# Kernel tuning notes

Measured on AMD Instinct MI355X. Metric: run time of the kernel, lower is better.

Reference implementation:

```python
import math
import jax, jax.numpy as jnp
from jax import lax
import numpy as np

BSZ, NQ, L, DM, DI, H, HD, DDIST, DCONV, DHID = 2, 128, 2048, 256, 512, 8, 64, 16, 4, 64
DKEY = DI * 2 + 2 + H  # key_proj output: z + xbc + per-head dt bias
DCV = DI + 2           # depthwise conv channels


def setup_inputs() -> dict:
    key = jax.random.key(0)
    ks = jax.random.split(key, 40)
    it = iter(range(40))
    def n(shape, s=1.0):
        return jax.random.normal(ks[next(it)], shape, jnp.float32) * s
    # dt_bias init exactly as in torch module
    dt = jnp.exp(jax.random.uniform(ks[next(it)], (H,)) * (math.log(0.1) - math.log(0.001)) + math.log(0.001))
    dt = jnp.maximum(dt, 1e-4)
    dt_bias = dt + jnp.log(-jnp.expm1(-dt))
    A_log = jnp.log(jax.random.uniform(ks[next(it)], (H,), minval=1.0, maxval=16.0))
    return {
        'queries': n((BSZ, NQ, DM)), 'anchors': n((BSZ, NQ, 3), 10.0),
        'features_perm': n((BSZ, L, DM)), 'pos_embed_perm': n((BSZ, L, DM)),
        'key_pos_3d': n((BSZ, L, 3), 10.0), 'query_pos': n((BSZ, NQ, DM)),
        'key_proj_w': n((DM, DKEY), 0.02),
        'key_conv_w': n((DCV, DCONV), 0.1), 'key_conv_b': jnp.zeros((DCV,)),
        'query_proj_w': n((DM, DI), 0.02),
        'dist_w1': n((3, DHID), 0.3), 'dist_b1': jnp.zeros((DHID,)), 'dist_w2': n((DHID, DDIST), 0.1),
        'bc_proj_w': n((DDIST, 2), 0.2), 'dt_proj_w': n((DDIST, H), 0.2),
        'dt_bias': dt_bias, 'A_log': A_log, 'D': jnp.ones((H,)),
        'key_norm_w': jnp.ones((DI,)), 'out_key_proj_w': n((DI, DM), 0.02),
        'query_norm_w': jnp.ones((DI,)), 'query_norm_b': jnp.zeros((DI,)),
        'out_query_proj_w': n((DI, DM), 0.02),
        'ffn_norm_w': jnp.ones((DM,)), 'ffn_norm_b': jnp.zeros((DM,)),
        'ffn_fc1_w': n((DM, 8 * DM), 0.02), 'ffn_fc1_b': jnp.zeros((8 * DM,)),
        'ffn_fc2_w': n((4 * DM, DM), 0.02), 'ffn_fc2_b': jnp.zeros((DM,)),
    }


def _ln(x, w, b, eps=1e-5):
    m = jnp.mean(x, -1, keepdims=True)
    v = jnp.mean((x - m) ** 2, -1, keepdims=True)
    return (x - m) * lax.rsqrt(v + eps) * w + b


def _dwconv_causal(x, w, b):
    # x [B,L,C], w [C,K]; torch pads K-1 both sides then slices [:L] == causal left pad
    lhs = jnp.swapaxes(x, 1, 2)  # [B,C,L]
    out = lax.conv_general_dilated(lhs, w[:, None, :], (1,), [(DCONV - 1, 0)],
                                   feature_group_count=w.shape[0],
                                   dimension_numbers=('NCH', 'OIH', 'NCH'))
    return jnp.swapaxes(out + b[None, :, None], 1, 2)


def _issm(x, dt, A, Bs, Cs, Dp, init):
    # x [B,L,H,P]; dt [B,L,H,N]; A [H,N]; Bs/Cs [B,L,N]; init [B,H,P,N]
    def step(h, inp):
        xt, dtt, bt, ct = inp  # [B,H,P], [B,H,N], [B,N], [B,N]
        h = h * jnp.exp(dtt * A)[:, :, None, :] + (dtt * bt[:, None, :])[:, :, None, :] * xt[..., None]
        return h, jnp.einsum('bhpn,bn->bhp', h, ct)
    xs = (jnp.swapaxes(x, 0, 1), jnp.swapaxes(dt, 0, 1), jnp.swapaxes(Bs, 0, 1), jnp.swapaxes(Cs, 0, 1))
    h_last, ys = lax.scan(step, init, xs)
    y = jnp.swapaxes(ys, 0, 1) + x * Dp[None, None, :, None]  # D skip inside scan, as in ISSM_chunk_scan_combined
    return y, h_last


def _forward(queries, anchors, features_perm, pos_embed_perm, key_pos_3d, query_pos,
             key_proj_w, key_conv_w, key_conv_b, query_proj_w, dist_w1, dist_b1, dist_w2,
             bc_proj_w, dt_proj_w, dt_bias, A_log, D, key_norm_w, out_key_proj_w,
             query_norm_w, query_norm_b, out_query_proj_w, ffn_norm_w, ffn_norm_b,
             ffn_fc1_w, ffn_fc1_b, ffn_fc2_w, ffn_fc2_b):
    qp = queries + query_pos
    kp = (features_perm + pos_embed_perm) @ key_proj_w            # [B,L,DKEY]
    z, xbc, dtb_seq = kp[..., :DI], kp[..., DI:DI + DCV], kp[..., DI + DCV:]
    xbc = jax.nn.silu(_dwconv_causal(xbc, key_conv_w, key_conv_b))
    x = xbc[..., :DI]
    b_bias, c_bias = xbc[..., DI], xbc[..., DI + 1]               # [B,L]
    init = (qp @ query_proj_w).reshape(BSZ, NQ, H, HD).transpose(0, 2, 3, 1)  # [B,H,HD,NQ]
    # distance features: delta [B,L,NQ,3]
    delta = anchors[:, None, :, :] - key_pos_3d[:, :, None, :]
    enc = jnp.sign(delta) * jnp.log2(jnp.abs(delta) * 20.0 + 1.0) / math.log2(8.0) / 4.0
    feat = jax.nn.relu(enc @ dist_w1 + dist_b1) @ dist_w2         # [B,L,NQ,DDIST]
    bc = feat @ bc_proj_w                                         # [B,L,NQ,2]
    Bssm = bc[..., 0] + b_bias[..., None]                         # [B,L,NQ]
    Cssm = bc[..., 1] + c_bias[..., None]
    dtb = jnp.swapaxes(feat @ dt_proj_w, 2, 3)                    # [B,L,H,NQ]
    dt = jax.nn.softplus(dtb + dtb_seq[..., None] + dt_bias[None, None, :, None])
    A = jnp.broadcast_to(-jnp.exp(A_log)[:, None], (H, NQ))
    xs = x.reshape(BSZ, L, H, HD)
    y_f, h_f = _issm(xs, dt, A, Bssm, Cssm, D, init)
    fl = lambda a: jnp.flip(a, axis=1)
    y_b, h_b = _issm(fl(xs), fl(dt), A, fl(Bssm), fl(Cssm), D, init)
    y = (y_f + fl(y_b)) * 0.5
    h = (h_f + h_b) * 0.5                                         # [B,H,HD,NQ]
    y = y.reshape(BSZ, L, DI) + x * jnp.repeat(D, HD)[None, None, :]
    # gated RMSNorm (norm_before_gate=False): gate first, then normalize
    g = y * jax.nn.silu(z)
    g = g * lax.rsqrt(jnp.mean(g * g, -1, keepdims=True) + 1e-5) * key_norm_w
    out_feat = features_perm + g @ out_key_proj_w
    hs = h.transpose(0, 3, 1, 2).reshape(BSZ, NQ, DI)             # b h hd n -> b n (h hd)
    out_q = queries + _ln(hs, query_norm_w, query_norm_b) @ out_query_proj_w
    fn = _ln(out_q, ffn_norm_w, ffn_norm_b)
    a, v = jnp.split(fn @ ffn_fc1_w + ffn_fc1_b, 2, axis=-1)
    out_q = out_q + (jax.nn.gelu(a, approximate=False) * v) @ ffn_fc2_w + ffn_fc2_b
    return out_q, out_feat


def reference(queries, anchors, features_perm, pos_embed_perm, key_pos_3d, query_pos,
              key_proj_w, key_conv_w, key_conv_b, query_proj_w, dist_w1, dist_b1, dist_w2,
              bc_proj_w, dt_proj_w, dt_bias, A_log, D, key_norm_w, out_key_proj_w,
              query_norm_w, query_norm_b, out_query_proj_w, ffn_norm_w, ffn_norm_b,
              ffn_fc1_w, ffn_fc1_b, ffn_fc2_w, ffn_fc2_b):
    return _forward(queries, anchors, features_perm, pos_embed_perm, key_pos_3d, query_pos,
                    key_proj_w, key_conv_w, key_conv_b, query_proj_w, dist_w1, dist_b1, dist_w2,
                    bc_proj_w, dt_proj_w, dt_bias, A_log, D, key_norm_w, out_key_proj_w,
                    query_norm_w, query_norm_b, out_query_proj_w, ffn_norm_w, ffn_norm_b,
                    ffn_fc1_w, ffn_fc1_b, ffn_fc2_w, ffn_fc2_b)
```

## Files before the change

### kernel.cpp

```cpp
#include <hip/hip_runtime.h>

typedef unsigned short u16;
typedef __bf16 bf16x8 __attribute__((ext_vector_type(8)));
typedef u16 u16x8 __attribute__((ext_vector_type(8)));
typedef float f32x4 __attribute__((ext_vector_type(4)));

#define BSZ_ 2
#define NQ_ 128
#define LSEQ_ 2048
#define DM_ 256
#define DI_ 512
#define NH_ 8
#define HD_ 64
#define DKEY_ 1034
#define DCV_ 514
#define NCHUNK_ 16
#define CT_ 128

__device__ __forceinline__ float bf2f(u16 u) {
  unsigned v = ((unsigned)u) << 16;
  return __builtin_bit_cast(float, v);
}
__device__ __forceinline__ u16 f2bf(float f) {
  unsigned u = __builtin_bit_cast(unsigned, f);
  u += 0x7fffu + ((u >> 16) & 1u);
  return (u16)(u >> 16);
}
__device__ __forceinline__ float sigmoidf_(float x) { return 1.f / (1.f + expf(-x)); }
__device__ __forceinline__ float softplusf_(float x) {
  return (x > 20.f) ? x : log1pf(expf(x));
}

template<bool F32>
__device__ __forceinline__ float ldi(const void* p, size_t i) {
  return F32 ? ((const float*)p)[i] : bf2f(((const u16*)p)[i]);
}
template<bool F32>
__device__ __forceinline__ void sto(void* p, size_t i, float v) {
  if (F32) ((float*)p)[i] = v;
  else ((u16*)p)[i] = f2bf(v);
}

__device__ __forceinline__ bool detect_f32(const void* feat) {
  int lane = threadIdx.x & 63;
  float a = fabsf(bf2f(((const u16*)feat)[2*lane]));
  bool plaus = (a > 1e-6f) && (a < 1e6f);
  unsigned long long m = __ballot(plaus);
  return __popcll(m) < 32;
}

constexpr size_t SZ_KP    = (size_t)BSZ_*LSEQ_*DKEY_;
constexpr size_t SZ_XACT  = (size_t)BSZ_*LSEQ_*DCV_;
constexpr size_t SZ_AW    = (size_t)BSZ_*NH_*LSEQ_*NQ_*2;
constexpr size_t SZ_CARR  = (size_t)BSZ_*LSEQ_*NQ_;
constexpr size_t SZ_QPROJ = (size_t)BSZ_*NQ_*DI_;
constexpr size_t SZ_YACC  = (size_t)BSZ_*LSEQ_*DI_;
constexpr size_t SZ_SEND  = (size_t)BSZ_*NH_*2*NCHUNK_*NQ_*HD_;
constexpr size_t SZ_PTOT  = (size_t)BSZ_*NH_*2*NCHUNK_*NQ_;
constexpr size_t SZ_H0    = SZ_SEND;
constexpr size_t SZ_HB    = (size_t)BSZ_*NH_*2*NQ_*HD_;
constexpr size_t SZ_GBUF  = (size_t)BSZ_*LSEQ_*DI_/2;
constexpr size_t SZ_OUTQF = (size_t)BSZ_*NQ_*DM_;
constexpr size_t SZ_WPREP = 2048;

constexpr size_t OFF_KP    = 0;
constexpr size_t OFF_XACT  = OFF_KP + SZ_KP;
constexpr size_t OFF_AW    = OFF_XACT + SZ_XACT;
constexpr size_t OFF_CARR  = OFF_AW + SZ_AW;
constexpr size_t OFF_QPROJ = OFF_CARR + SZ_CARR;
constexpr size_t OFF_YACC  = OFF_QPROJ + SZ_QPROJ;
constexpr size_t OFF_SEND  = OFF_YACC + SZ_YACC;
constexpr size_t OFF_PTOT  = OFF_SEND + SZ_SEND;
constexpr size_t OFF_H0    = OFF_PTOT + SZ_PTOT;
constexpr size_t OFF_HB    = OFF_H0 + SZ_H0;
constexpr size_t OFF_GBUF  = OFF_HB + SZ_HB;
constexpr size_t OFF_OUTQF = OFF_GBUF + SZ_GBUF;
constexpr size_t OFF_WPREP = OFF_OUTQF + SZ_OUTQF;
constexpr size_t WS_FLOATS = OFF_WPREP + SZ_WPREP;

constexpr size_t OFF_UG  = OFF_AW;
constexpr size_t OFF_LNQ = OFF_UG + (size_t)256*1024/2;
constexpr size_t OFF_LNF = OFF_LNQ + (size_t)256*512/2;

constexpr size_t OFF_ABUF = OFF_SEND;
constexpr size_t OFF_AQ   = OFF_ABUF + (size_t)4096*256/2;
constexpr size_t OFF_BKEY = OFF_AQ + (size_t)256*256/2;
constexpr size_t OFF_BQ   = OFF_BKEY + (size_t)(256*1034+1)/2 + 1;
constexpr size_t OFF_BOK  = OFF_SEND;
constexpr size_t OFF_BOQ  = OFF_BOK + (size_t)512*256/2;
constexpr size_t OFF_B1W  = OFF_BOQ + (size_t)512*256/2;
constexpr size_t OFF_B2W  = OFF_B1W + (size_t)256*2048/2;

template<bool F32>
__device__ void prep_body(const void* A_log, const void* dt_bias,
                          const void* w1, const void* b1, const void* w2,
                          const void* bcw, const void* dtw, float* wp) {
  int t = threadIdx.x;
  if (t < 8) {
    wp[t]     = -expf(ldi<F32>(A_log, t));
    wp[8 + t] = ldi<F32>(dt_bias, t);
  }
  if (t < 64) {
    wp[32 + t*4 + 0] = ldi<F32>(w1, 0*64 + t);
    wp[32 + t*4 + 1] = ldi<F32>(w1, 1*64 + t);
    wp[32 + t*4 + 2] = ldi<F32>(w1, 2*64 + t);
    wp[32 + t*4 + 3] = ldi<F32>(b1, t);
  }
  for (int i = t; i < 1024; i += 256) wp[288 + i] = ldi<F32>(w2, i);
  if (t < 32)  wp[1312 + t] = ldi<F32>(bcw, t);
  if (t < 128) wp[1344 + t] = ldi<F32>(dtw, t);
}

__device__ __forceinline__ void cast_job(bool F32, const void* s0, const void* s1_,
                                         u16* d, size_t n, size_t base, size_t stride) {
  for (size_t i = base; i < n; i += stride) {
    float v = F32 ? ((const float*)s0)[i] : bf2f(((const u16*)s0)[i]);
    if (s1_) v += F32 ? ((const float*)s1_)[i] : bf2f(((const u16*)s1_)[i]);
    d[i] = f2bf(v);
  }
}

__global__ __launch_bounds__(256) void setup_kernel(
    const void* feat, const void* pe, u16* abuf,
    const void* q, const void* qp, u16* aq,
    const void* kw, u16* bkey, const void* qw, u16* bq,
    const void* A_log, const void* dt_bias, const void* w1, const void* b1,
    const void* w2, const void* bcw, const void* dtw, float* wp,
    float* yacc, int* flag)
{
  int bx = blockIdx.x, tid = threadIdx.x;
  if (bx < 512) {
    size_t base = (size_t)bx * 4096 + tid;
#pragma unroll
    for (int k = 0; k < 16; ++k) yacc[base + (size_t)k*256] = 0.f;
    return;
  }
  bool F32 = detect_f32(feat);
  if (bx < 1024) {
    cast_job(F32, feat, pe, abuf, (size_t)4096*256,
             (size_t)(bx-512)*256 + tid, (size_t)512*256);
  } else if (bx < 1056) {
    cast_job(F32, q, qp, aq, (size_t)256*256,
             (size_t)(bx-1024)*256 + tid, (size_t)32*256);
  } else if (bx < 1184) {
    cast_job(F32, kw, nullptr, bkey, (size_t)256*1034,
             (size_t)(bx-1056)*256 + tid, (size_t)128*256);
  } else if (bx < 1248) {
    cast_job(F32, qw, nullptr, bq, (size_t)256*512,
             (size_t)(bx-1184)*256 + tid, (size_t)64*256);
  } else {
    if (tid == 0) *flag = F32 ? 1 : 0;
    if (F32) prep_body<true>(A_log, dt_bias, w1, b1, w2, bcw, dtw, wp);
    else     prep_body<false>(A_log, dt_bias, w1, b1, w2, bcw, dtw, wp);
  }
}

template<int A_MODE, int B_MODE, int OUT_EXT, int RES_EXT, int RES_F32, int BIAS, bool F32>
__device__ void gemm_body(int bm, int bn,
                          const void* A0, const void* A1, const void* Bw,
                          float* Cf, void* Cext, const void* ResE,
                          const float* ResF, const void* Bias,
                          int M, int N, int K) {
  __shared__ u16 As[64][40];
  __shared__ u16 Bs[64][42];
  int tid = threadIdx.x;
  int w = tid >> 6, lane = tid & 63;
  f32x4 acc[4];
#pragma unroll
  for (int j = 0; j < 4; ++j) acc[j] = (f32x4){0.f, 0.f, 0.f, 0.f};

  int arow = tid >> 2, aseg = (tid & 3) * 8;
  int bkl = tid >> 3, bns = (tid & 7) * 8;

  for (int k0 = 0; k0 < K; k0 += 32) {
    {
      size_t abase = (size_t)(bm + arow) * K + k0 + aseg;
      u16x8 tv;
      if (A_MODE == 0) {
#pragma unroll
        for (int i = 0; i < 8; ++i)
          tv[i] = f2bf(ldi<F32>(A0, abase + i) + ldi<F32>(A1, abase + i));
      } else {
        const u16* pa = (const u16*)A0 + abase;
#pragma unroll
        for (int i = 0; i < 8; ++i) tv[i] = pa[i];
      }
      *(u16x8*)&As[arow][aseg] = tv;
    }
    {
      size_t bbase = (size_t)(k0 + bkl) * N + bn + bns;
#pragma unroll
      for (int i = 0; i < 8; ++i) {
        u16 v;
        if (bn + bns + i < N) {
          if (B_MODE == 1) v = ((const u16*)Bw)[bbase + i];
          else             v = f2bf(ldi<F32>(Bw, bbase + i));
        } else v = (u16)0;
        Bs[bns + i][bkl] = v;
      }
    }
    __syncthreads();
    int mrow = w * 16 + (lane & 15);
    int kq = (lane >> 4) * 8;
    bf16x8 af = __builtin_bit_cast(bf16x8, *(const u16x8*)&As[mrow][kq]);
#pragma unroll
    for (int j = 0; j < 4; ++j) {
      bf16x8 bfv = __builtin_bit_cast(bf16x8, *(const u16x8*)&Bs[j*16 + (lane & 15)][kq]);
      acc[j] = __builtin_amdgcn_mfma_f32_16x16x32_bf16(af, bfv, acc[j], 0, 0, 0);
    }
    __syncthreads();
  }
  int col0 = lane & 15, rbase = (lane >> 4) * 4;
#pragma unroll
  for (int j = 0; j < 4; ++j) {
#pragma unroll
    for (int r = 0; r < 4; ++r) {
      int row = bm + w * 16 + rbase + r;
      int col = bn + j * 16 + col0;
      if (col < N) {
        size_t idx = (size_t)row * N + col;
        float v = acc[j][r];
        if (BIAS)    v += ldi<F32>(Bias, col);
        if (RES_EXT) v += ldi<F32>(ResE, idx);
        if (RES_F32) v += ResF[idx];
        if (OUT_EXT) sto<F32>(Cext, idx, v);
        else         Cf[idx] = v;
      }
    }
  }
}

__global__ __launch_bounds__(256) void kp_gemm_kernel(
    const u16* abuf, const u16* bkey, float* kp) {
  gemm_body<1,1,0,0,0,0,false>(blockIdx.x*64, blockIdx.y*64, abuf, nullptr, bkey,
                               kp, nullptr, nullptr, nullptr, nullptr,
                               4096, DKEY_, DM_);
}

template<bool F32>
__device__ void fc2_body(const u16* ug, const u16* b2w, void* out_q,
                         const float* outqf, const void* b2) {
  gemm_body<1,1,1,0,1,1,F32>((blockIdx.x&3)*64, (blockIdx.x>>2)*64, ug, nullptr,
                             b2w, nullptr, out_q, nullptr, outqf, b2,
                             BSZ_*NQ_, DM_, 1024);
}
__global__ __launch_bounds__(256) void fc2_kernel(
    const int* fl, const u16* ug, const u16* b2w, void* out_q,
    const float* outqf, const void* b2) {
  if (*fl) fc2_body<true>(ug, b2w, out_q, outqf, b2);
  else     fc2_body<false>(ug, b2w, out_q, outqf, b2);
}

template<bool F32>
__device__ void conv_body(const float* kp, const void* cw, const void* cb,
                          float* xact) {
  int row = blockIdx.x;
  int l = row & (LSEQ_ - 1);
  for (int ch = threadIdx.x; ch < DCV_; ch += 256) {
    float acc = ldi<F32>(cb, ch);
#pragma unroll
    for (int k = 0; k < 4; ++k) {
      int ll = l - 3 + k;
      if (ll >= 0)
        acc = fmaf(ldi<F32>(cw, ch*4 + k), kp[(size_t)(row - 3 + k)*DKEY_ + DI_ + ch], acc);
    }
    xact[(size_t)row*DCV_ + ch] = acc * sigmoidf_(acc);
  }
}
__global__ __launch_bounds__(256) void convqp_kernel(
    const int* fl, const float* kp, const void* cw, const void* cb, float* xact,
    const u16* aq, const u16* bq, float* qproj)
{
  int bx = blockIdx.x;
  if (bx < 4096) {
    if (*fl) conv_body<true>(kp, cw, cb, xact);
    else     conv_body<false>(kp, cw, cb, xact);
  } else {
    int i = bx - 4096;
    gemm_body<1,1,0,0,0,0,false>((i&3)*64, (i>>2)*64, aq, nullptr, bq,
                                 qproj, nullptr, nullptr, nullptr, nullptr,
                                 BSZ_*NQ_, DI_, DM_);
  }
}

template<bool F32>
__device__ void dist_body(const void* anchors, const void* key_pos,
                          const float* kp, const float* xact, const float* wp,
                          float* aw, float* carr) {
  int tid = threadIdx.x;
  int n = tid & 127;
  int idx = blockIdx.x;
  int b = idx >> 10;
  int l = ((idx & 1023) << 1) | (tid >> 7);
  size_t row = (size_t)b * LSEQ_ + l;

  float enc0, enc1, enc2;
  {
    float e[3];
#pragma unroll
    for (int d = 0; d < 3; ++d) {
      float delta = ldi<F32>(anchors, (b*NQ_ + n)*3 + d) - ldi<F32>(key_pos, row*3 + d);
      float s = delta < 0.f ? -1.f : 1.f;
      e[d] = s * log2f(fabsf(delta) * 20.f + 1.f) * (1.f/12.f);
    }
    enc0 = e[0]; enc1 = e[1]; enc2 = e[2];
  }
  float feat[16];
#pragma unroll
  for (int f = 0; f < 16; ++f) feat[f] = 0.f;
  for (int j = 0; j < 64; ++j) {
    float w0 = wp[32 + j*4], w1v = wp[33 + j*4], w2v = wp[34 + j*4], bb = wp[35 + j*4];
    float hj = fmaxf(fmaf(enc0, w0, fmaf(enc1, w1v, fmaf(enc2, w2v, bb))), 0.f);
#pragma unroll
    for (int f = 0; f < 16; ++f) feat[f] = fmaf(hj, wp[288 + j*16 + f], feat[f]);
  }
  float bc0 = 0.f, bc1 = 0.f;
#pragma unroll
  for (int f = 0; f < 16; ++f) {
    bc0 = fmaf(feat[f], wp[1312 + f*2], bc0);
    bc1 = fmaf(feat[f], wp[1313 + f*2], bc1);
  }
  float bb_ = xact[row*DCV_ + DI_];
  float cb_ = xact[row*DCV_ + DI_ + 1];
  float Bs = bc0 + bb_, Cs = bc1 + cb_;
  carr[row*NQ_ + n] = Cs;

  float dtb[8];
#pragma unroll
  for (int h = 0; h < 8; ++h) dtb[h] = 0.f;
#pragma unroll
  for (int f = 0; f < 16; ++f)
#pragma unroll
    for (int h = 0; h < 8; ++h) dtb[h] = fmaf(feat[f], wp[1344 + f*8 + h], dtb[h]);

#pragma unroll
  for (int h = 0; h < 8; ++h) {
    float xln = dtb[h] + kp[row*DKEY_ + (DI_*2 + 2) + h] + wp[8 + h];
    float dtv = softplusf_(xln);
    float a = expf(dtv * wp[h]);
    float wv = dtv * Bs;
    size_t o = (((size_t)(b*NH_ + h)*LSEQ_ + l)*NQ_ + n)*2;
    aw[o] = a;
    aw[o + 1] = wv;
  }
}
__global__ __launch_bounds__(256) void dist_kernel(
    const int* fl, const void* anchors, const void* key_pos, const float* kp,
    const float* xact, const float* wp, float* aw, float* carr) {
  if (*fl) dist_body<true>(anchors, key_pos, kp, xact, wp, aw, carr);
  else     dist_body<false>(anchors, key_pos, kp, xact, wp, aw, carr);
}

__global__ __launch_bounds__(256) void s1m_kernel(
    const float* __restrict__ aw, const float* __restrict__ xact,
    float* __restrict__ send, float* __restrict__ ptot)
{
  int tid = threadIdx.x;
  int hd = tid & 63;
  int w = __builtin_amdgcn_readfirstlane(tid >> 6);
  int ns = blockIdx.x, q = blockIdx.y, z = blockIdx.z;
  int h = z & 7, b = z >> 3;
  int n0 = __builtin_amdgcn_readfirstlane(ns*16 + w*4);

  float hf[4], hb[4], pr[4];
#pragma unroll
  for (int i = 0; i < 4; ++i) { hf[i] = 0.f; hb[i] = 0.f; pr[i] = 1.f; }

  size_t awbase = (size_t)z * LSEQ_ * (NQ_*2);
  int t = q*CT_;
  for (int s = 0; s < CT_; ++s, ++t) {
    const float* awt = aw + awbase + (size_t)t*(NQ_*2) + n0*2;
    float xv = xact[((size_t)(b*LSEQ_ + t))*DCV_ + (h << 6) + hd];
#pragma unroll
    for (int i = 0; i < 4; ++i) {
      float a = awt[2*i], wv = awt[2*i + 1];
      float wx = wv * xv;
      hf[i] = fmaf(hf[i], a, wx);
      hb[i] = fmaf(pr[i], wx, hb[i]);
      pr[i] *= a;
    }
  }
  size_t cbf = (size_t)((z*2 + 0)*NCHUNK_ + q);
  size_t cbb = (size_t)((z*2 + 1)*NCHUNK_ + (NCHUNK_ - 1 - q));
#pragma unroll
  for (int i = 0; i < 4; ++i) {
    send[cbf*(NQ_*HD_) + (size_t)(n0 + i)*HD_ + hd] = hf[i];
    send[cbb*(NQ_*HD_) + (size_t)(n0 + i)*HD_ + hd] = hb[i];
  }
  if (hd == 0) {
#pragma unroll
    for (int i = 0; i < 4; ++i) {
      ptot[cbf*NQ_ + n0 + i] = pr[i];
      ptot[cbb*NQ_ + n0 + i] = pr[i];
    }
  }
}

__global__ __launch_bounds__(256) void s2_kernel(
    const float* __restrict__ qproj, const float* __restrict__ ptot,
    const float* __restrict__ send, float* __restrict__ h0buf,
    float* __restrict__ hbuf)
{
  int g = blockIdx.x*256 + threadIdx.x;
  int hd = g & 63;
  int n = (g >> 6) & 127;
  int dir = (g >> 13) & 1;
  int h = (g >> 14) & 7;
  int b = g >> 17;
  float hcur = qproj[((size_t)(b*NQ_ + n))*DI_ + h*HD_ + hd];
  size_t base = (size_t)((b*NH_ + h)*2 + dir) * NCHUNK_;
  for (int q = 0; q < NCHUNK_; ++q) {
    size_t cb = base + q;
    h0buf[cb*(NQ_*HD_) + (size_t)n*HD_ + hd] = hcur;
    hcur = fmaf(hcur, ptot[cb*NQ_ + n], send[cb*(NQ_*HD_) + (size_t)n*HD_ + hd]);
  }
  hbuf[((size_t)((b*NH_ + h)*2 + dir))*(NQ_*HD_) + (size_t)n*HD_ + hd] = hcur;
}

template<bool F32>
__device__ void cast1_part(const void* okw, u16* bok, const void* oqw, u16* boq,
                           const void* w1, u16* b1w, const void* w2, u16* b2w) {
  int i = blockIdx.x - 2048;
  int job = i >> 7, bj = i & 127;
  size_t base = (size_t)bj*256 + threadIdx.x, stride = (size_t)128*256;
  switch (job) {
    case 0: cast_job(F32, okw, nullptr, bok, (size_t)512*256, base, stride); break;
    case 1: cast_job(F32, oqw, nullptr, boq, (size_t)512*256, base, stride); break;
    case 2: cast_job(F32, w1, nullptr, b1w, (size_t)256*2048, base, stride); break;
    default: cast_job(F32, w2, nullptr, b2w, (size_t)1024*256, base, stride); break;
  }
}
__global__ __launch_bounds__(256) void s3cast_kernel(
    const int* fl, const float* __restrict__ aw, const float* __restrict__ carr,
    const float* __restrict__ xact, const float* __restrict__ h0buf,
    float* __restrict__ yacc,
    const void* okw, u16* bok, const void* oqw, u16* boq,
    const void* w1, u16* b1w, const void* w2, u16* b2w)
{
  int bx = blockIdx.x;
  if (bx >= 2048) {
    if (*fl) cast1_part<true>(okw, bok, oqw, boq, w1, b1w, w2, b2w);
    else     cast1_part<false>(okw, bok, oqw, boq, w1, b1w, w2, b2w);
    return;
  }
  int tid = threadIdx.x;
  int hd = tid & 63;
  int w = __builtin_amdgcn_readfirstlane(tid >> 6);
  int ns = bx & 3, q = (bx >> 2) & 15, zz = bx >> 6;
  int dir = zz & 1, h = (zz >> 1) & 7, b = zz >> 4;
  int n0 = __builtin_amdgcn_readfirstlane(ns*32 + w*8);

  float hst[8];
  size_t cb = (size_t)(((b*NH_ + h)*2 + dir)*NCHUNK_ + q);
#pragma unroll
  for (int i = 0; i < 8; ++i)
    hst[i] = h0buf[cb*(NQ_*HD_) + (size_t)(n0 + i)*HD_ + hd];

  __shared__ float ybuf[2][4][64];
  size_t awbase = (size_t)(b*NH_ + h) * LSEQ_ * (NQ_*2);
  int tbase = dir ? (LSEQ_ - 1 - q*CT_) : (q*CT_);
  int tstep = dir ? -1 : 1;
  int t = tbase;
  for (int s = 0; s < CT_; ++s, t += tstep) {
    const float* awt = aw + awbase + (size_t)t*(NQ_*2) + n0*2;
    const float* ct = carr + ((size_t)(b*LSEQ_ + t))*NQ_ + n0;
    float xv = xact[((size_t)(b*LSEQ_ + t))*DCV_ + (h << 6) + hd];
    float ys = 0.f;
#pragma unroll
    for (int i = 0; i < 8; ++i) {
      hst[i] = fmaf(hst[i], awt[2*i], awt[2*i + 1] * xv);
      ys = fmaf(hst[i], ct[i], ys);
    }
    int p = s & 1;
    ybuf[p][w][hd] = ys;
    __syncthreads();
    if (w == 0) {
      float yv = ybuf[p][0][hd] + ybuf[p][1][hd] + ybuf[p][2][hd] + ybuf[p][3][hd];
      atomicAdd(&yacc[((size_t)(b*LSEQ_ + t))*DI_ + (h << 6) + hd], 0.5f * yv);
    }
  }
}

__device__ __forceinline__ float block_sum256(float v, float* red) {
#pragma unroll
  for (int off = 32; off; off >>= 1) v += __shfl_xor(v, off, 64);
  int wv = threadIdx.x >> 6;
  if ((threadIdx.x & 63) == 0) red[wv] = v;
  __syncthreads();
  float t = red[0] + red[1] + red[2] + red[3];
  __syncthreads();
  return t;
}

template<bool F32>
__device__ void g_body(const float* yacc, const float* xact, const float* kp,
                       const void* Dv, const void* knw, u16* gbuf) {
  int row = blockIdx.x, tid = threadIdx.x;
  __shared__ float red[4];
  float gg[2];
  float ss = 0.f;
#pragma unroll
  for (int ii = 0; ii < 2; ++ii) {
    int ch = tid + ii*256;
    float yv = yacc[(size_t)row*DI_ + ch];
    float xv = xact[(size_t)row*DCV_ + ch];
    float zv = kp[(size_t)row*DKEY_ + ch];
    float Dh = ldi<F32>(Dv, ch >> 6);
    float yf = yv + 2.f * Dh * xv;
    float g = yf * (zv * sigmoidf_(zv));
    gg[ii] = g;
    ss += g * g;
  }
  float tot = block_sum256(ss, red);
  float r = rsqrtf(tot / (float)DI_ + 1e-5f);
#pragma unroll
  for (int ii = 0; ii < 2; ++ii) {
    int ch = tid + ii*256;
    gbuf[(size_t)row*DI_ + ch] = f2bf(gg[ii] * r * ldi<F32>(knw, ch));
  }
}
template<bool F32>
__device__ void lnq_body(const float* hbuf, const void* qnw, const void* qnb,
                         u16* lnq) {
  int row = blockIdx.x - 4096;
  int b = row >> 7, n = row & 127;
  int tid = threadIdx.x;
  __shared__ float red[4];
  float hv[2];
  float s1 = 0.f, s2 = 0.f;
#pragma unroll
  for (int ii = 0; ii < 2; ++ii) {
    int ch = tid + ii*256;
    int h = ch >> 6, hd = ch & 63;
    size_t base = ((size_t)((b*NH_ + h)*2))*(NQ_*HD_) + (size_t)n*HD_ + hd;
    float v = 0.5f * (hbuf[base] + hbuf[base + (size_t)NQ_*HD_]);
    hv[ii] = v;
    s1 += v;
    s2 += v * v;
  }
  s1 = block_sum256(s1, red);
  s2 = block_sum256(s2, red);
  float mean = s1 / (float)DI_;
  float var = fmaxf(s2 / (float)DI_ - mean * mean, 0.f);
  float rstd = rsqrtf(var + 1e-5f);
#pragma unroll
  for (int ii = 0; ii < 2; ++ii) {
    int ch = tid + ii*256;
    lnq[(size_t)row*DI_ + ch] =
        f2bf((hv[ii] - mean) * rstd * ldi<F32>(qnw, ch) + ldi<F32>(qnb, ch));
  }
}
__global__ __launch_bounds__(256) void glnq_kernel(
    const int* fl, const float* yacc, const float* xact, const float* kp,
    const void* Dv, const void* knw, u16* gbuf,
    const float* hbuf, const void* qnw, const void* qnb, u16* lnq)
{
  if (blockIdx.x < 4096) {
    if (*fl) g_body<true>(yacc, xact, kp, Dv, knw, gbuf);
    else     g_body<false>(yacc, xact, kp, Dv, knw, gbuf);
  } else {
    if (*fl) lnq_body<true>(hbuf, qnw, qnb, lnq);
    else     lnq_body<false>(hbuf, qnw, qnb, lnq);
  }
}

template<bool F32>
__device__ void ofoq_body(const u16* gbuf, const u16* bok, void* out_feat,
                          const void* features, const u16* lnq, const u16* boq,
                          float* outqf, const void* queries) {
  int bx = blockIdx.x;
  if (bx < 256) {
    gemm_body<1,1,1,1,0,0,F32>((bx>>2)*64, (bx&3)*64, gbuf, nullptr, bok,
                               nullptr, out_feat, features, nullptr, nullptr,
                               4096, DM_, DI_);
  } else {
    int i = bx - 256;
    gemm_body<1,1,0,1,0,0,F32>((i&3)*64, (i>>2)*64, lnq, nullptr, boq,
                               outqf, nullptr, queries, nullptr, nullptr,
                               BSZ_*NQ_, DM_, DI_);
  }
}
__global__ __launch_bounds__(256) void ofoq_kernel(
    const int* fl, const u16* gbuf, const u16* bok,
    void* out_feat_f32, void* out_feat_bf16, const void* features,
    const u16* lnq, const u16* boq, float* outqf, const void* queries) {
  if (*fl) ofoq_body<true>(gbuf, bok, out_feat_f32, features, lnq, boq, outqf, queries);
  else     ofoq_body<false>(gbuf, bok, out_feat_bf16, features, lnq, boq, outqf, queries);
}

template<bool F32>
__device__ void lnf_body(const float* outqf, const void* fnw, const void* fnb,
                         u16* lnf) {
  int row = blockIdx.x, tid = threadIdx.x;
  __shared__ float red[4];
  float x = outqf[(size_t)row*DM_ + tid];
  float s1 = block_sum256(x, red);
  float s2 = block_sum256(x * x, red);
  float mean = s1 / (float)DM_;
  float var = fmaxf(s2 / (float)DM_ - mean * mean, 0.f);
  float rstd = rsqrtf(var + 1e-5f);
  lnf[(size_t)row*DM_ + tid] =
      f2bf((x - mean) * rstd * ldi<F32>(fnw, tid) + ldi<F32>(fnb, tid));
}
__global__ __launch_bounds__(256) void lnf_kernel(
    const int* fl, const float* outqf, const void* fnw, const void* fnb, u16* lnf) {
  if (*fl) lnf_body<true>(outqf, fnw, fnb, lnf);
  else     lnf_body<false>(outqf, fnw, fnb, lnf);
}

template<bool F32>
__device__ void fc1g_body(const u16* lnf, const u16* b1w, const void* b1, u16* ug) {
  __shared__ u16 As[64][40];
  __shared__ u16 BsA[64][42];
  __shared__ u16 BsV[64][42];
  int tid = threadIdx.x;
  int w = tid >> 6, lane = tid & 63;
  int bm = blockIdx.x * 64, bn = blockIdx.y * 64;
  f32x4 accA[4], accV[4];
#pragma unroll
  for (int j = 0; j < 4; ++j) {
    accA[j] = (f32x4){0.f, 0.f, 0.f, 0.f};
    accV[j] = (f32x4){0.f, 0.f, 0.f, 0.f};
  }
  int arow = tid >> 2, aseg = (tid & 3) * 8;
  int bkl = tid >> 3, bns = (tid & 7) * 8;

  for (int k0 = 0; k0 < DM_; k0 += 32) {
    {
      size_t abase = (size_t)(bm + arow) * DM_ + k0 + aseg;
      const u16* pa = lnf + abase;
      u16x8 tv;
#pragma unroll
      for (int i = 0; i < 8; ++i) tv[i] = pa[i];
      *(u16x8*)&As[arow][aseg] = tv;
    }
    {
      size_t bbase = (size_t)(k0 + bkl) * 2048 + bn + bns;
#pragma unroll
      for (int i = 0; i < 8; ++i) {
        BsA[bns + i][bkl] = b1w[bbase + i];
        BsV[bns + i][bkl] = b1w[bbase + 1024 + i];
      }
    }
    __syncthreads();
    int mrow = w * 16 + (lane & 15);
    int kq = (lane >> 4) * 8;
    bf16x8 af = __builtin_bit_cast(bf16x8, *(const u16x8*)&As[mrow][kq]);
#pragma unroll
    for (int j = 0; j < 4; ++j) {
      bf16x8 ba = __builtin_bit_cast(bf16x8, *(const u16x8*)&BsA[j*16 + (lane & 15)][kq]);
      bf16x8 bv = __builtin_bit_cast(bf16x8, *(const u16x8*)&BsV[j*16 + (lane & 15)][kq]);
      accA[j] = __builtin_amdgcn_mfma_f32_16x16x32_bf16(af, ba, accA[j], 0, 0, 0);
      accV[j] = __builtin_amdgcn_mfma_f32_16x16x32_bf16(af, bv, accV[j], 0, 0, 0);
    }
    __syncthreads();
  }
  int col0 = lane & 15, rbase = (lane >> 4) * 4;
#pragma unroll
  for (int j = 0; j < 4; ++j) {
#pragma unroll
    for (int r = 0; r < 4; ++r) {
      int row = bm + w * 16 + rbase + r;
      int col = bn + j * 16 + col0;
      float a = accA[j][r] + ldi<F32>(b1, col);
      float v = accV[j][r] + ldi<F32>(b1, col + 1024);
      float ge = 0.5f * a * (1.f + erff(a * 0.70710678118f));
      ug[(size_t)row*1024 + col] = f2bf(ge * v);
    }
  }
}
__global__ __launch_bounds__(256) void fc1g_kernel(
    const int* fl, const u16* lnf, const u16* b1w, const void* b1, u16* ug) {
  if (*fl) fc1g_body<true>(lnf, b1w, b1, ug);
  else     fc1g_body<false>(lnf, b1w, b1, ug);
}

extern "C" void kernel_launch(void* const* d_in, const int* in_sizes, int n_in,
                              void* d_out, int out_size, void* d_ws, size_t ws_size,
                              hipStream_t stream) {
  const void* queries        = d_in[0];
  const void* anchors        = d_in[1];
  const void* features       = d_in[2];
  const void* pos_embed      = d_in[3];
  const void* key_pos        = d_in[4];
  const void* query_pos      = d_in[5];
  const void* key_proj_w     = d_in[6];
  const void* key_conv_w     = d_in[7];
  const void* key_conv_b     = d_in[8];
  const void* query_proj_w   = d_in[9];
  const void* dist_w1        = d_in[10];
  const void* dist_b1        = d_in[11];
  const void* dist_w2        = d_in[12];
  const void* bc_proj_w      = d_in[13];
  const void* dt_proj_w      = d_in[14];
  const void* dt_bias        = d_in[15];
  const void* A_log          = d_in[16];
  const void* Dvec           = d_in[17];
  const void* key_norm_w     = d_in[18];
  const void* out_key_proj_w = d_in[19];
  const void* query_norm_w   = d_in[20];
  const void* query_norm_b   = d_in[21];
  const void* out_query_proj_w = d_in[22];
  const void* ffn_norm_w     = d_in[23];
  const void* ffn_norm_b     = d_in[24];
  const void* ffn_fc1_w      = d_in[25];
  const void* ffn_fc1_b      = d_in[26];
  const void* ffn_fc2_w      = d_in[27];
  const void* ffn_fc2_b      = d_in[28];

  if (ws_size < WS_FLOATS * sizeof(float)) return;

  float* ws    = (float*)d_ws;
  float* kp    = ws + OFF_KP;
  float* xact  = ws + OFF_XACT;
  float* aw    = ws + OFF_AW;
  float* carr  = ws + OFF_CARR;
  float* qproj = ws + OFF_QPROJ;
  float* yacc  = ws + OFF_YACC;
  float* send  = ws + OFF_SEND;
  float* ptot  = ws + OFF_PTOT;
  float* h0buf = ws + OFF_H0;
  float* hbuf  = ws + OFF_HB;
  u16*   gbuf  = (u16*)(ws + OFF_GBUF);
  float* outqf = ws + OFF_OUTQF;
  float* wprep = ws + OFF_WPREP;
  int*   flag  = (int*)(wprep + 1536);
  u16*   ugbuf = (u16*)(ws + OFF_UG);
  u16*   lnq   = (u16*)(ws + OFF_LNQ);
  u16*   lnf   = (u16*)(ws + OFF_LNF);
  u16*   abuf  = (u16*)(ws + OFF_ABUF);
  u16*   aq    = (u16*)(ws + OFF_AQ);
  u16*   bkey  = (u16*)(ws + OFF_BKEY);
  u16*   bq    = (u16*)(ws + OFF_BQ);
  u16*   bok   = (u16*)(ws + OFF_BOK);
  u16*   boq   = (u16*)(ws + OFF_BOQ);
  u16*   b1w   = (u16*)(ws + OFF_B1W);
  u16*   b2w   = (u16*)(ws + OFF_B2W);

  void* out_q = d_out;
  void* out_feat_bf16 = (void*)((u16*)d_out + (size_t)BSZ_*NQ_*DM_);
  void* out_feat_f32  = (void*)((float*)d_out + (size_t)BSZ_*NQ_*DM_);

  setup_kernel<<<1249, 256, 0, stream>>>(
      features, pos_embed, abuf, queries, query_pos, aq,
      key_proj_w, bkey, query_proj_w, bq,
      A_log, dt_bias, dist_w1, dist_b1, dist_w2, bc_proj_w, dt_proj_w, wprep,
      yacc, flag);

  kp_gemm_kernel<<<dim3(64, 17), 256, 0, stream>>>(abuf, bkey, kp);

  convqp_kernel<<<4096 + 32, 256, 0, stream>>>(
      flag, kp, key_conv_w, key_conv_b, xact, aq, bq, qproj);

  dist_kernel<<<BSZ_*LSEQ_/2, 256, 0, stream>>>(flag, anchors, key_pos, kp, xact,
                                                wprep, aw, carr);

  s1m_kernel<<<dim3(8, NCHUNK_, BSZ_*NH_), 256, 0, stream>>>(aw, xact, send, ptot);

  s2_kernel<<<1024, 256, 0, stream>>>(qproj, ptot, send, h0buf, hbuf);

  s3cast_kernel<<<2048 + 512, 256, 0, stream>>>(
      flag, aw, carr, xact, h0buf, yacc,
      out_key_proj_w, bok, out_query_proj_w, boq, ffn_fc1_w, b1w, ffn_fc2_w, b2w);

  glnq_kernel<<<4096 + 256, 256, 0, stream>>>(
      flag, yacc, xact, kp, Dvec, key_norm_w, gbuf,
      hbuf, query_norm_w, query_norm_b, lnq);

  ofoq_kernel<<<256 + 16, 256, 0, stream>>>(
      flag, gbuf, bok, out_feat_f32, out_feat_bf16, features,
      lnq, boq, outqf, queries);

  lnf_kernel<<<BSZ_*NQ_, 256, 0, stream>>>(flag, outqf, ffn_norm_w, ffn_norm_b, lnf);

  fc1g_kernel<<<dim3(4, 16), 256, 0, stream>>>(flag, lnf, b1w, ffn_fc1_b, ugbuf);

  fc2_kernel<<<16, 256, 0, stream>>>(flag, ugbuf, b2w, out_q, outqf, ffn_fc2_b);
}
```

Measured before the change: 436.2 us.

## Fuse forward and backward scan chunks per block and accumulate outputs in shared memory

Each s3 block now handles the forward and the backward direction for the same time chunk together, which halves the block count and gives two independent FMA chains per step. The per-step __syncthreads and global atomicAdd are replaced by shared-memory atomic accumulation into a 128x64 buffer, written to yacc with global atomics once at the end. This removes 128 barriers per block and cuts global atomics, at the cost of 32KB of LDS per block, which may lower occupancy, plus LDS atomic contention among the four waves.

```diff
diff --git a/kernel.cpp b/kernel.cpp
--- a/kernel.cpp
+++ b/kernel.cpp
@@ -420,7 +420,7 @@
 template<bool F32>
 __device__ void cast1_part(const void* okw, u16* bok, const void* oqw, u16* boq,
                            const void* w1, u16* b1w, const void* w2, u16* b2w) {
-  int i = blockIdx.x - 2048;
+  int i = blockIdx.x - 1024;
   int job = i >> 7, bj = i & 127;
   size_t base = (size_t)bj*256 + threadIdx.x, stride = (size_t)128*256;
   switch (job) {
@@ -438,46 +438,66 @@
     const void* w1, u16* b1w, const void* w2, u16* b2w)
 {
   int bx = blockIdx.x;
-  if (bx >= 2048) {
+  if (bx >= 1024) {
     if (*fl) cast1_part<true>(okw, bok, oqw, boq, w1, b1w, w2, b2w);
     else     cast1_part<false>(okw, bok, oqw, boq, w1, b1w, w2, b2w);
     return;
   }
+  __shared__ float ybuf[CT_ * 64];
   int tid = threadIdx.x;
   int hd = tid & 63;
   int w = __builtin_amdgcn_readfirstlane(tid >> 6);
-  int ns = bx & 3, q = (bx >> 2) & 15, zz = bx >> 6;
-  int dir = zz & 1, h = (zz >> 1) & 7, b = zz >> 4;
+  int ns = bx & 3, c = (bx >> 2) & 15, h = (bx >> 6) & 7, b = bx >> 9;
+  int z = b*NH_ + h;
   int n0 = __builtin_amdgcn_readfirstlane(ns*32 + w*8);
 
-  float hst[8];
-  size_t cb = (size_t)(((b*NH_ + h)*2 + dir)*NCHUNK_ + q);
-#pragma unroll
-  for (int i = 0; i < 8; ++i)
-    hst[i] = h0buf[cb*(NQ_*HD_) + (size_t)(n0 + i)*HD_ + hd];
-
-  __shared__ float ybuf[2][4][64];
-  size_t awbase = (size_t)(b*NH_ + h) * LSEQ_ * (NQ_*2);
-  int tbase = dir ? (LSEQ_ - 1 - q*CT_) : (q*CT_);
-  int tstep = dir ? -1 : 1;
-  int t = tbase;
-  for (int s = 0; s < CT_; ++s, t += tstep) {
-    const float* awt = aw + awbase + (size_t)t*(NQ_*2) + n0*2;
-    const float* ct = carr + ((size_t)(b*LSEQ_ + t))*NQ_ + n0;
-    float xv = xact[((size_t)(b*LSEQ_ + t))*DCV_ + (h << 6) + hd];
-    float ys = 0.f;
+#pragma unroll
+  for (int k = 0; k < 32; ++k) ybuf[k*256 + tid] = 0.f;
+
+  float hf[8], hb[8];
+  size_t cbf = (size_t)((z*2 + 0)*NCHUNK_ + c);
+  size_t cbb = (size_t)((z*2 + 1)*NCHUNK_ + (NCHUNK_ - 1 - c));
+#pragma unroll
+  for (int i = 0; i < 8; ++i) {
+    hf[i] = h0buf[cbf*(NQ_*HD_) + (size_t)(n0 + i)*HD_ + hd];
+    hb[i] = h0buf[cbb*(NQ_*HD_) + (size_t)(n0 + i)*HD_ + hd];
+  }
+  __syncthreads();
+
+  size_t awbase = (size_t)z * LSEQ_ * (NQ_*2);
+  int tf = c*CT_;
+  int tb = c*CT_ + CT_ - 1;
+  const float* awf = aw + awbase + (size_t)tf*(NQ_*2) + n0*2;
+  const float* awb = aw + awbase + (size_t)tb*(NQ_*2) + n0*2;
+  const float* ctf = carr + ((size_t)(b*LSEQ_) + tf)*NQ_ + n0;
+  const float* ctb = carr + ((size_t)(b*LSEQ_) + tb)*NQ_ + n0;
+  const float* xaf = xact + ((size_t)(b*LSEQ_) + tf)*DCV_ + (h << 6) + hd;
+  const float* xab = xact + ((size_t)(b*LSEQ_) + tb)*DCV_ + (h << 6) + hd;
+
+  for (int s = 0; s < CT_; ++s) {
+    float xvf = *xaf, xvb = *xab;
+    float ysf = 0.f, ysb = 0.f;
 #pragma unroll
     for (int i = 0; i < 8; ++i) {
-      hst[i] = fmaf(hst[i], awt[2*i], awt[2*i + 1] * xv);
-      ys = fmaf(hst[i], ct[i], ys);
-    }
-    int p = s & 1;
-    ybuf[p][w][hd] = ys;
-    __syncthreads();
-    if (w == 0) {
-      float yv = ybuf[p][0][hd] + ybuf[p][1][hd] + ybuf[p][2][hd] + ybuf[p][3][hd];
-      atomicAdd(&yacc[((size_t)(b*LSEQ_ + t))*DI_ + (h << 6) + hd], 0.5f * yv);
-    }
+      hf[i] = fmaf(hf[i], awf[2*i], awf[2*i + 1] * xvf);
+      ysf = fmaf(hf[i], ctf[i], ysf);
+      hb[i] = fmaf(hb[i], awb[2*i], awb[2*i + 1] * xvb);
+      ysb = fmaf(hb[i], ctb[i], ysb);
+    }
+    atomicAdd(&ybuf[s*64 + hd], ysf);
+    atomicAdd(&ybuf[(CT_ - 1 - s)*64 + hd], ysb);
+    awf += NQ_*2; awb -= NQ_*2;
+    ctf += NQ_;   ctb -= NQ_;
+    xaf += DCV_;  xab -= DCV_;
+  }
+  __syncthreads();
+
+  size_t ybase = ((size_t)(b*LSEQ_) + c*CT_)*DI_ + (h << 6);
+#pragma unroll
+  for (int k = 0; k < 32; ++k) {
+    int idx = k*256 + tid;
+    int s = idx >> 6, hh = idx & 63;
+    atomicAdd(&yacc[ybase + (size_t)s*DI_ + hh], 0.5f * ybuf[idx]);
   }
 }
 
@@ -759,7 +779,7 @@
 
   s2_kernel<<<1024, 256, 0, stream>>>(qproj, ptot, send, h0buf, hbuf);
 
-  s3cast_kernel<<<2048 + 512, 256, 0, stream>>>(
+  s3cast_kernel<<<1024 + 512, 256, 0, stream>>>(
       flag, aw, carr, xact, h0buf, yacc,
       out_key_proj_w, bok, out_query_proj_w, boq, ffn_fc1_w, b1w, ffn_fc2_w, b2w);
 
```

Result: slower. 685.7 us (+57.2%).
